# Kernel tuning notes

Hardware: AMD Instinct MI355X
Metric: run time of the kernel (lower is better)

Reference implementation:

```python
import jax, jax.numpy as jnp
import numpy as np

N_NODES = 50000
N_EDGES = 800000
N_GRAPHS = 128
IN_CH = 31
HID = 64
EPS = 1e-5


def _glorot(key, shape, scale=0.05):
    return jax.random.normal(key, shape, dtype=jnp.float32) * scale


def setup_inputs() -> dict:
    key = jax.random.key(0)
    ks = jax.random.split(key, 16)
    x = jax.random.normal(ks[0], (N_NODES, IN_CH), dtype=jnp.float32)
    edge_index = jax.random.randint(ks[1], (2, N_EDGES), 0, N_NODES, dtype=jnp.int32)
    batch = jnp.sort(jax.random.randint(ks[2], (N_NODES,), 0, N_GRAPHS, dtype=jnp.int32))
    params = {
        "t": jnp.ones((1,), dtype=jnp.float32),  # shared learnable softmax temperature
        "W1r": _glorot(ks[3], (HID, IN_CH)), "b1": jnp.zeros((HID,), jnp.float32), "W1s": _glorot(ks[4], (HID, IN_CH)),
        "W2r": _glorot(ks[5], (HID, HID)),  "b2": jnp.zeros((HID,), jnp.float32), "W2s": _glorot(ks[6], (HID, HID)),
        "W3r": _glorot(ks[7], (HID, HID)),  "b3": jnp.zeros((HID,), jnp.float32), "W3s": _glorot(ks[8], (HID, HID)),
        "Wl1": _glorot(ks[9], (2 * HID, 3 * HID)), "bl1": jnp.zeros((2 * HID,), jnp.float32),
        "Wl2": _glorot(ks[10], (HID // 2, 2 * HID)), "bl2": jnp.zeros((HID // 2,), jnp.float32),
    }
    return {"x": x, "edge_index": edge_index, "batch": batch, **params}


def _softmax_aggr(m, dst, t, n):
    # segment-softmax over incoming edges, per channel: alpha = softmax(t*m | dst)
    logits = m * t  # [E, C]
    mx = jax.ops.segment_max(logits, dst, num_segments=n)  # [N, C]
    e = jnp.exp(logits - mx[dst])
    denom = jax.ops.segment_sum(e, dst, num_segments=n)
    alpha = e / denom[dst]
    return jax.ops.segment_sum(m * alpha, dst, num_segments=n)  # [N, C]


def _graph_conv(x, src, dst, t, Wr, br, Ws):
    # PyG GraphConv: out = lin_rel(aggr_j x_j) + lin_root(x); lin_root has no bias
    m = x[src]  # gather [E, C]
    aggr = _softmax_aggr(m, dst, t, x.shape[0])
    return aggr @ Wr.T + br + x @ Ws.T


def _instance_norm(x):
    # torch InstanceNorm1d on [N, C] input -> normalize each row over feature dim
    mu = jnp.mean(x, axis=1, keepdims=True)
    var = jnp.mean((x - mu) ** 2, axis=1, keepdims=True)
    return (x - mu) / jnp.sqrt(var + EPS)


def reference(x, edge_index, batch, t, W1r, b1, W1s, W2r, b2, W2s, W3r, b3, W3s, Wl1, bl1, Wl2, bl2):
    src, dst = edge_index[0], edge_index[1]
    x1 = jax.nn.relu(_instance_norm(_graph_conv(x, src, dst, t, W1r, b1, W1s)))
    x2 = jax.nn.relu(_instance_norm(_graph_conv(x1, src, dst, t, W2r, b2, W2s)))
    x3 = jax.nn.relu(_instance_norm(_graph_conv(x2, src, dst, t, W3r, b3, W3s)))
    h1 = jax.ops.segment_max(x1, batch, num_segments=N_GRAPHS)
    h2 = jax.ops.segment_max(x2, batch, num_segments=N_GRAPHS)
    h3 = jax.ops.segment_max(x3, batch, num_segments=N_GRAPHS)
    h = jnp.concatenate([h1, h2, h3], axis=1)  # [G, 3*HID]
    z = jax.nn.relu(h @ Wl1.T + bl1)  # dropout is identity in eval mode
    z = z @ Wl2.T + bl2
    norm = jnp.maximum(jnp.linalg.norm(z, axis=1, keepdims=True), 1e-12)
    return z / norm
```

## Files before the change

### kernel.cpp

```cpp
#include <hip/hip_runtime.h>
#include <hip/hip_fp16.h>

#define N_NODES 50000
#define N_EDGES 800000
#define N_GRAPHS 128
#define IN_CH 31
#define HID 64

typedef __attribute__((ext_vector_type(8))) short short8;
typedef __attribute__((ext_vector_type(8))) unsigned short ushort8;
typedef __attribute__((ext_vector_type(4))) float floatx4;
typedef __attribute__((ext_vector_type(8))) _Float16 half8;

__device__ inline unsigned short f2h(float f) {
    __half h = __float2half_rn(f);
    return __half_as_ushort(h);
}
__device__ inline unsigned packh2(float a, float b) {
    __half2 h = __floats2half2_rn(a, b);
    return *(unsigned*)&h;
}
__device__ inline void pack4h(short* p, float4 v) {
    unsigned lo = packh2(v.x, v.y);
    unsigned hi = packh2(v.z, v.w);
    *(uint2*)p = make_uint2(lo, hi);
}
__device__ inline unsigned packEP(float E, float P) {
    return packh2(E, P);
}
__device__ inline float2 unpackEP(unsigned u) {
    __half2 h = *(__half2*)&u;
    return __half22float2(h);
}

__global__ void prep_kernel(const float* __restrict__ x, const float* __restrict__ tptr,
                            unsigned short* __restrict__ xh, unsigned* __restrict__ EP0,
                            int nN) {
    int i = blockIdx.x * 256 + threadIdx.x;
    if (i >= nN * 32) return;
    int node = i >> 5, c = i & 31;
    if (c < IN_CH) {
        float xv = x[node * IN_CH + c];
        xh[node * IN_CH + c] = f2h(xv);
        float tval = tptr[0];
        float E = __expf(tval * xv);
        EP0[i] = packEP(E, xv * E);
    } else {
        EP0[i] = 0;
    }
}


#define BKT_SHIFT 7
#define BKT_MAX 512
#define CHUNK 8192
#define CAP 2560

__global__ void bucket_scatter_kernel(const int* __restrict__ src,
                                      const int* __restrict__ dst,
                                      int* __restrict__ bucket_cnt,
                                      unsigned* __restrict__ ebuf, int e, int nb) {
    __shared__ int bins[BKT_MAX];
    __shared__ int base[BKT_MAX];
    __shared__ int lcur[BKT_MAX];
    int tid = threadIdx.x;
    int i0 = blockIdx.x * CHUNK;
    int i1 = i0 + CHUNK; if (i1 > e) i1 = e;
    for (int k = tid; k < nb; k += 256) { bins[k] = 0; lcur[k] = 0; }
    __syncthreads();
    for (int j = i0 + tid; j < i1; j += 256)
        atomicAdd(&bins[dst[j] >> BKT_SHIFT], 1);
    __syncthreads();
    for (int k = tid; k < nb; k += 256)
        if (bins[k]) base[k] = atomicAdd(&bucket_cnt[k], bins[k]);
    __syncthreads();
    for (int j = i0 + tid; j < i1; j += 256) {
        int ss = src[j], dd = dst[j];
        int b = dd >> BKT_SHIFT;
        int p = atomicAdd(&lcur[b], 1);
        ebuf[(size_t)b * CAP + base[b] + p] = (unsigned)ss | ((unsigned)(dd & 127) << 16);
    }
}

__global__ void bucket_csr_kernel(const unsigned* __restrict__ ebuf,
                                  const int* __restrict__ bucket_cnt,
                                  int* __restrict__ row_ptr, int* __restrict__ deg,
                                  int* __restrict__ csr_src, int nN) {
    __shared__ int nh[128];
    __shared__ int s[128];
    __shared__ int ncur[128];
    int tid = threadIdx.x;
    int b = blockIdx.x;
    int cnt = bucket_cnt[b];
    size_t boff = (size_t)b * CAP;
    int node0 = b << BKT_SHIFT;
    if (tid < 128) nh[tid] = 0;
    __syncthreads();
    for (int j = tid; j < cnt; j += 256)
        atomicAdd(&nh[ebuf[boff + j] >> 16], 1);
    __syncthreads();
    int v = (tid < 128) ? nh[tid] : 0;
    if (tid < 128) s[tid] = v;
    __syncthreads();
    for (int off = 1; off < 128; off <<= 1) {
        int u = (tid < 128 && tid >= off) ? s[tid - off] : 0;
        __syncthreads();
        if (tid < 128) s[tid] += u;
        __syncthreads();
    }
    if (tid < 128 && node0 + tid < nN) {
        int excl = (int)boff + s[tid] - v;
        row_ptr[node0 + tid] = excl;
        deg[node0 + tid] = v;
        ncur[tid] = excl;
    }
    __syncthreads();
    for (int j = tid; j < cnt; j += 256) {
        unsigned ed = ebuf[boff + j];
        int pos = atomicAdd(&ncur[ed >> 16], 1);
        csr_src[pos] = (int)(ed & 0xFFFF);
    }
}


template <int C_IN>
__global__ void __launch_bounds__(256, 8) aggr_kernel(
        const unsigned* __restrict__ EP, const unsigned short* __restrict__ xin,
        const float* __restrict__ tptr,
        const int* __restrict__ row_ptr, const int* __restrict__ deg,
        const int* __restrict__ csr_src,
        unsigned short* __restrict__ aRowsB, int n) {
    int w = threadIdx.x >> 6, l = threadIdx.x & 63;
    int d = blockIdx.x * 4 + w;
    if (d >= n) return;
    int beg = __builtin_amdgcn_readfirstlane(row_ptr[d]);
    int dg  = __builtin_amdgcn_readfirstlane(deg[d]);
    int end = beg + dg;
    int half = l >> 5;

    if constexpr (C_IN == 64) {
        int co = l & 31;
        float t2 = tptr[0] * 1.44269504f;
        const unsigned* Y = (const unsigned*)xin;
        float2 num2 = {0.f, 0.f}, den2 = {0.f, 0.f};
        int base = beg;
        for (; base + 64 <= end; base += 64) {
            int sidx = csr_src[base + l];
            #pragma unroll
            for (int j = 0; j < 64; j += 16) {
                unsigned v[8];
                #pragma unroll
                for (int p = 0; p < 8; ++p) {
                    int sa = __builtin_amdgcn_readlane(sidx, j + 2 * p);
                    int sb = __builtin_amdgcn_readlane(sidx, j + 2 * p + 1);
                    int s  = half ? sb : sa;
                    v[p] = Y[(size_t)s * 32 + co];
                }
                #pragma unroll
                for (int p = 0; p < 8; ++p) {
                    float2 y = __half22float2(*(__half2*)&v[p]);
                    float E0 = exp2f(t2 * y.x);
                    float E1 = exp2f(t2 * y.y);
                    den2.x += E0; num2.x = fmaf(y.x, E0, num2.x);
                    den2.y += E1; num2.y = fmaf(y.y, E1, num2.y);
                }
            }
        }
        int rem = end - base;
        if (rem > 0) {
            int sidx = csr_src[base + ((l < rem) ? l : 0)];
            for (int j = 0; j < rem; j += 16) {
                unsigned v[8];
                #pragma unroll
                for (int p = 0; p < 8; ++p) {
                    int ja = j + 2 * p;     if (ja >= rem) ja = rem - 1;
                    int jb = j + 2 * p + 1; if (jb >= rem) jb = rem - 1;
                    int sa = __builtin_amdgcn_readlane(sidx, ja);
                    int sb = __builtin_amdgcn_readlane(sidx, jb);
                    int s  = half ? sb : sa;
                    v[p] = Y[(size_t)s * 32 + co];
                }
                #pragma unroll
                for (int p = 0; p < 8; ++p) {
                    float m = (j + 2 * p + half < rem) ? 1.f : 0.f;
                    float2 y = __half22float2(*(__half2*)&v[p]);
                    float E0 = exp2f(t2 * y.x);
                    float E1 = exp2f(t2 * y.y);
                    den2.x = fmaf(E0, m, den2.x); num2.x = fmaf(y.x * E0, m, num2.x);
                    den2.y = fmaf(E1, m, den2.y); num2.y = fmaf(y.y * E1, m, num2.y);
                }
            }
        }
        num2.x += __shfl_xor(num2.x, 32);
        num2.y += __shfl_xor(num2.y, 32);
        den2.x += __shfl_xor(den2.x, 32);
        den2.y += __shfl_xor(den2.y, 32);
        float nx = __shfl(num2.x, l >> 1);
        float ny = __shfl(num2.y, l >> 1);
        float dx = __shfl(den2.x, l >> 1);
        float dy = __shfl(den2.y, l >> 1);
        float num = (l & 1) ? ny : nx;
        float den = (l & 1) ? dy : dx;
        float aggr = (dg > 0 && den > 0.f) ? num / den : 0.f;
        aRowsB[(size_t)d * 64 + l] = f2h(aggr);
    } else {
        int ch = l & 31;
        int chc = (ch < C_IN) ? ch : (C_IN - 1);
        float num = 0.f, den = 0.f;
        int base = beg;
        for (; base + 64 <= end; base += 64) {
            int sidx = csr_src[base + l];
            #pragma unroll
            for (int j = 0; j < 64; j += 16) {
                unsigned v[8];
                #pragma unroll
                for (int p = 0; p < 8; ++p) {
                    int sa = __builtin_amdgcn_readlane(sidx, j + 2 * p);
                    int sb = __builtin_amdgcn_readlane(sidx, j + 2 * p + 1);
                    int s  = half ? sb : sa;
                    v[p] = EP[(size_t)s * 32 + chc];
                }
                #pragma unroll
                for (int p = 0; p < 8; ++p) {
                    float2 e = unpackEP(v[p]);
                    den += e.x;
                    num += e.y;
                }
            }
        }
        int rem = end - base;
        if (rem > 0) {
            int sidx = csr_src[base + ((l < rem) ? l : 0)];
            for (int j = 0; j < rem; j += 16) {
                unsigned v[8];
                #pragma unroll
                for (int p = 0; p < 8; ++p) {
                    int ja = j + 2 * p;     if (ja >= rem) ja = rem - 1;
                    int jb = j + 2 * p + 1; if (jb >= rem) jb = rem - 1;
                    int sa = __builtin_amdgcn_readlane(sidx, ja);
                    int sb = __builtin_amdgcn_readlane(sidx, jb);
                    int s  = half ? sb : sa;
                    v[p] = EP[(size_t)s * 32 + chc];
                }
                #pragma unroll
                for (int p = 0; p < 8; ++p) {
                    float m = (j + 2 * p + half < rem) ? 1.f : 0.f;
                    float2 e = unpackEP(v[p]);
                    den = fmaf(e.x, m, den);
                    num = fmaf(e.y, m, num);
                }
            }
        }
        num += __shfl_xor(num, 32);
        den += __shfl_xor(den, 32);
        float aggr = (dg > 0 && den > 0.f) ? num / den : 0.f;
        unsigned short outv;
        if (l < C_IN)               outv = f2h(aggr);
        else if (l < 2 * C_IN)      outv = xin[(size_t)d * C_IN + (l - C_IN)];
        else                        outv = 0;
        aRowsB[(size_t)d * 64 + l] = outv;
    }
}


template <int C_IN, bool WY>
__global__ void __launch_bounds__(256, 4) transform_kernel(
        const unsigned short* __restrict__ aRowsB, const unsigned short* __restrict__ yprev,
        const int* __restrict__ batch,
        const float* __restrict__ Wr, const float* __restrict__ br,
        const float* __restrict__ Ws,
        unsigned short* __restrict__ yout,
        float* __restrict__ hmax, int n) {
    constexpr int K_TOT = (C_IN == 64) ? 128 : 64;
    constexpr int KP    = K_TOT + 8;
    constexpr int KS    = K_TOT / 32;
    constexpr int ABSH  = 2 * 64 * KP;
    constexpr int CSH   = 64 * 68 * 2;
    constexpr int SMSH  = (ABSH > CSH) ? ABSH : CSH;

    __shared__ short smem[SMSH];
    short* sA = smem;
    short* sB = smem + 64 * KP;
    float* sC = (float*)smem;

    int tid = threadIdx.x;
    int nb = blockIdx.x * 64;

    if constexpr (C_IN == 64) {
        for (int idx = tid; idx < 64 * 16; idx += 256) {
            int row = idx >> 4, c8 = idx & 15;
            int node = nb + row; if (node >= n) node = n - 1;
            ushort8 v = (c8 < 8) ? ((const ushort8*)(aRowsB + (size_t)node * 64))[c8]
                                 : ((const ushort8*)(yprev + (size_t)node * 64))[c8 - 8];
            *(ushort8*)&sA[row * KP + c8 * 8] = v;
        }
        for (int idx = tid; idx < 64 * 32; idx += 256) {
            int nr = idx >> 5, c4 = idx & 31;
            float4 v = (c4 < 16) ? ((const float4*)(Wr + nr * 64))[c4]
                                 : ((const float4*)(Ws + nr * 64))[c4 - 16];
            pack4h(&sB[nr * KP + c4 * 4], v);
        }
    } else {
        for (int idx = tid; idx < 64 * 8; idx += 256) {
            int row = idx >> 3, c8 = idx & 7;
            int node = nb + row; if (node >= n) node = n - 1;
            ushort8 v = ((const ushort8*)(aRowsB + (size_t)node * 64))[c8];
            *(ushort8*)&sA[row * KP + c8 * 8] = v;
        }
        for (int idx = tid; idx < 64 * 64; idx += 256) {
            int nr = idx >> 6, k = idx & 63;
            float v = (k < C_IN) ? Wr[nr * C_IN + k]
                    : (k < 2 * C_IN) ? Ws[nr * C_IN + (k - C_IN)] : 0.f;
            sB[nr * KP + k] = (short)f2h(v);
        }
    }
    __syncthreads();

    int w = tid >> 6, l = tid & 63;
    int m = l & 15;
    int q = l >> 4;
    floatx4 acc[4] = {{0.f,0.f,0.f,0.f},{0.f,0.f,0.f,0.f},
                      {0.f,0.f,0.f,0.f},{0.f,0.f,0.f,0.f}};
    const short* aBase = &sA[(w * 16 + m) * KP + q * 8];
    #pragma unroll 2
    for (int s = 0; s < KS; ++s) {
        half8 af = *(const half8*)(aBase + s * 32);
        #pragma unroll
        for (int t = 0; t < 4; ++t) {
            half8 bf = *(const half8*)&sB[(t * 16 + m) * KP + q * 8 + s * 32];
            acc[t] = __builtin_amdgcn_mfma_f32_16x16x32_f16(af, bf, acc[t], 0, 0, 0);
        }
    }

    __syncthreads();
    #pragma unroll
    for (int t = 0; t < 4; ++t)
        #pragma unroll
        for (int r = 0; r < 4; ++r)
            sC[(w * 16 + q * 4 + r) * 68 + t * 16 + m] = acc[t][r];
    __syncthreads();

    float bias = br[l];
    int gcur = -1;
    float rmax = 0.f;
    for (int i = 0; i < 16; ++i) {
        int j = w * 16 + i;
        int d = nb + j;
        if (d < n) {
            float a = sC[j * 68 + l] + bias;
            float s = a;
            for (int off = 32; off > 0; off >>= 1) s += __shfl_xor(s, off);
            float mu = s * (1.0f / 64.0f);
            float dc = a - mu;
            float s2 = dc * dc;
            for (int off = 32; off > 0; off >>= 1) s2 += __shfl_xor(s2, off);
            float var = s2 * (1.0f / 64.0f);
            float y = dc * rsqrtf(var + 1e-5f);
            y = fmaxf(y, 0.f);
            if constexpr (WY) {
                yout[(size_t)d * 64 + l] = f2h(y);
            }
            int g = __builtin_amdgcn_readfirstlane(batch[d]);
            if (g != gcur) {
                if (gcur >= 0)
                    atomicMax((int*)&hmax[gcur * 64 + l], __float_as_int(rmax));
                gcur = g;
                rmax = 0.f;
            }
            rmax = fmaxf(rmax, y);
        }
    }
    if (gcur >= 0)
        atomicMax((int*)&hmax[gcur * 64 + l], __float_as_int(rmax));
}


__global__ void mlp_kernel(const float* __restrict__ h,
                           const float* __restrict__ Wl1, const float* __restrict__ bl1,
                           const float* __restrict__ Wl2, const float* __restrict__ bl2,
                           float* __restrict__ out) {
    __shared__ float hrow[192];
    __shared__ float z1[128];
    __shared__ float z2[32];
    __shared__ float snorm;
    int g = blockIdx.x, tid = threadIdx.x;
    if (tid < 64) {
        hrow[tid]       = h[0 * N_GRAPHS * 64 + g * 64 + tid];
        hrow[64 + tid]  = h[1 * N_GRAPHS * 64 + g * 64 + tid];
        hrow[128 + tid] = h[2 * N_GRAPHS * 64 + g * 64 + tid];
    }
    __syncthreads();
    float acc = bl1[tid];
    #pragma unroll 8
    for (int c = 0; c < 192; ++c) acc = fmaf(hrow[c], Wl1[tid * 192 + c], acc);
    z1[tid] = fmaxf(acc, 0.f);
    __syncthreads();
    if (tid < 32) {
        float a2 = bl2[tid];
        #pragma unroll 8
        for (int c = 0; c < 128; ++c) a2 = fmaf(z1[c], Wl2[tid * 128 + c], a2);
        z2[tid] = a2;
    }
    __syncthreads();
    if (tid == 0) {
        float ss = 0.f;
        for (int i = 0; i < 32; ++i) ss += z2[i] * z2[i];
        snorm = fmaxf(sqrtf(ss), 1e-12f);
    }
    __syncthreads();
    if (tid < 32) out[g * 32 + tid] = z2[tid] / snorm;
}


extern "C" void kernel_launch(void* const* d_in, const int* in_sizes, int n_in,
                              void* d_out, int out_size, void* d_ws, size_t ws_size,
                              hipStream_t stream) {
    const float* x   = (const float*)d_in[0];
    const int* eidx  = (const int*)d_in[1];
    const int* batch = (const int*)d_in[2];
    const float* t   = (const float*)d_in[3];
    const float* W1r = (const float*)d_in[4];
    const float* b1  = (const float*)d_in[5];
    const float* W1s = (const float*)d_in[6];
    const float* W2r = (const float*)d_in[7];
    const float* b2  = (const float*)d_in[8];
    const float* W2s = (const float*)d_in[9];
    const float* W3r = (const float*)d_in[10];
    const float* b3  = (const float*)d_in[11];
    const float* W3s = (const float*)d_in[12];
    const float* Wl1 = (const float*)d_in[13];
    const float* bl1 = (const float*)d_in[14];
    const float* Wl2 = (const float*)d_in[15];
    const float* bl2 = (const float*)d_in[16];
    float* out = (float*)d_out;

    const int nE = in_sizes[1] / 2;
    const int nN = in_sizes[2];
    const int* src = eidx;
    const int* dst = eidx + nE;
    const int nb = (nN + 127) >> BKT_SHIFT;

    char* ws = (char*)d_ws;
    size_t off = 0;
    auto alloc = [&](size_t bytes) {
        char* p = ws + off;
        off = (off + bytes + 255) & ~(size_t)255;
        return p;
    };
    int*            bucket_cnt = (int*)alloc((size_t)BKT_MAX * 4);
    float*          h          = (float*)alloc((size_t)3 * N_GRAPHS * 64 * 4);
    int*            row_ptr    = (int*)alloc((size_t)nN * 4);
    int*            deg        = (int*)alloc((size_t)nN * 4);
    unsigned*       ebuf       = (unsigned*)alloc((size_t)nb * CAP * 4);
    int*            csr_src    = (int*)alloc((size_t)nb * CAP * 4);
    unsigned short* xh         = (unsigned short*)alloc((size_t)nN * IN_CH * 2);
    unsigned*       EP0        = (unsigned*)alloc((size_t)nN * 32 * 4);
    unsigned short* yAh        = (unsigned short*)alloc((size_t)nN * 64 * 2);
    unsigned short* yBh        = (unsigned short*)alloc((size_t)nN * 64 * 2);
    unsigned short* aRowsB     = (unsigned short*)alloc((size_t)nN * 64 * 2);

    const int nbChunk = (nE + CHUNK - 1) / CHUNK;

    hipMemsetAsync(bucket_cnt, 0,
                   (char*)(h + 3 * N_GRAPHS * 64) - (char*)bucket_cnt, stream);
    prep_kernel<<<(nN * 32 + 255) / 256, 256, 0, stream>>>(x, t, xh, EP0, nN);
    bucket_scatter_kernel<<<nbChunk, 256, 0, stream>>>(src, dst, bucket_cnt, ebuf, nE, nb);
    bucket_csr_kernel<<<nb, 256, 0, stream>>>(ebuf, bucket_cnt, row_ptr, deg, csr_src, nN);

    const int nbA = (nN + 3) / 4;
    const int nbT = (nN + 63) / 64;

    aggr_kernel<IN_CH><<<nbA, 256, 0, stream>>>(EP0, xh, t, row_ptr, deg, csr_src, aRowsB, nN);
    transform_kernel<IN_CH, true><<<nbT, 256, 0, stream>>>(
        aRowsB, nullptr, batch, W1r, b1, W1s, yAh, h + 0 * N_GRAPHS * 64, nN);

    aggr_kernel<HID><<<nbA, 256, 0, stream>>>(nullptr, yAh, t, row_ptr, deg, csr_src, aRowsB, nN);
    transform_kernel<HID, true><<<nbT, 256, 0, stream>>>(
        aRowsB, yAh, batch, W2r, b2, W2s, yBh, h + 1 * N_GRAPHS * 64, nN);

    aggr_kernel<HID><<<nbA, 256, 0, stream>>>(nullptr, yBh, t, row_ptr, deg, csr_src, aRowsB, nN);
    transform_kernel<HID, false><<<nbT, 256, 0, stream>>>(
        aRowsB, yBh, batch, W3r, b3, W3s, nullptr, h + 2 * N_GRAPHS * 64, nN);

    mlp_kernel<<<N_GRAPHS, 128, 0, stream>>>(h, Wl1, bl1, Wl2, bl2, out);
}
```

Measured before the change: 295.2 us.

## Precompute per-node exp and weighted values in transform epilogue for layers 2-3

The transform kernel now writes, for each node and channel, a packed fp16 pair of exp(t*y) and y*exp(t*y) alongside y. The 64-channel aggregation then gathers these precomputed pairs instead of recomputing exp per edge. The aggregation loop is unified into one generic path with 8-edge batches, one source node per load, and fdot2-based masked accumulation. The intent is to remove per-edge exp work, at the cost of doubling the gathered bytes per edge (4 bytes per channel instead of 2) and losing the two-edges-per-wave interleave.

```diff
diff --git a/kernel.cpp b/kernel.cpp
--- a/kernel.cpp
+++ b/kernel.cpp
@@ -11,6 +11,11 @@
 typedef __attribute__((ext_vector_type(8))) unsigned short ushort8;
 typedef __attribute__((ext_vector_type(4))) float floatx4;
 typedef __attribute__((ext_vector_type(8))) _Float16 half8;
+typedef __attribute__((ext_vector_type(2))) _Float16 half2v;
+
+#if __has_builtin(__builtin_amdgcn_fdot2)
+#define HAS_FDOT2 1
+#endif
 
 __device__ inline unsigned short f2h(float f) {
     __half h = __float2half_rn(f);
@@ -31,6 +36,9 @@
 __device__ inline float2 unpackEP(unsigned u) {
     __half2 h = *(__half2*)&u;
     return __half22float2(h);
+}
+__device__ inline half2v u2h2(unsigned u) {
+    return __builtin_bit_cast(half2v, u);
 }
 
 __global__ void prep_kernel(const float* __restrict__ x, const float* __restrict__ tptr,
@@ -126,134 +134,64 @@
 template <int C_IN>
 __global__ void __launch_bounds__(256, 8) aggr_kernel(
         const unsigned* __restrict__ EP, const unsigned short* __restrict__ xin,
-        const float* __restrict__ tptr,
         const int* __restrict__ row_ptr, const int* __restrict__ deg,
         const int* __restrict__ csr_src,
         unsigned short* __restrict__ aRowsB, int n) {
+    constexpr int ROWD = (C_IN == 64) ? 64 : 32;
     int w = threadIdx.x >> 6, l = threadIdx.x & 63;
     int d = blockIdx.x * 4 + w;
     if (d >= n) return;
     int beg = __builtin_amdgcn_readfirstlane(row_ptr[d]);
     int dg  = __builtin_amdgcn_readfirstlane(deg[d]);
     int end = beg + dg;
-    int half = l >> 5;
+    int cl = l & (ROWD - 1);
+
+    float den0 = 0.f, den1 = 0.f, num0 = 0.f, num1 = 0.f;
+    for (int base = beg; base < end; base += 64) {
+        int cend = base + 64; if (cend > end) cend = end;
+        int chunk = cend - base;
+        int sidx = csr_src[base + ((l < chunk) ? l : 0)];
+        for (int j0 = 0; j0 < chunk; j0 += 8) {
+            int jc = chunk - j0;
+            unsigned v[8];
+            #pragma unroll
+            for (int p = 0; p < 8; ++p) {
+                int jj = (p < jc) ? (j0 + p) : (chunk - 1);
+                int s  = __builtin_amdgcn_readlane(sidx, jj);
+                v[p] = EP[(size_t)s * ROWD + cl];
+            }
+            #pragma unroll
+            for (int p = 0; p < 8; ++p) {
+                bool live = (p < jc);
+#ifdef HAS_FDOT2
+                unsigned bE = live ? 0x00003C00u : 0u;
+                unsigned bP = live ? 0x3C000000u : 0u;
+                if (p & 1) {
+                    den1 = __builtin_amdgcn_fdot2(u2h2(v[p]), u2h2(bE), den1, false);
+                    num1 = __builtin_amdgcn_fdot2(u2h2(v[p]), u2h2(bP), num1, false);
+                } else {
+                    den0 = __builtin_amdgcn_fdot2(u2h2(v[p]), u2h2(bE), den0, false);
+                    num0 = __builtin_amdgcn_fdot2(u2h2(v[p]), u2h2(bP), num0, false);
+                }
+#else
+                float mm = live ? 1.f : 0.f;
+                float2 e = unpackEP(v[p]);
+                if (p & 1) {
+                    den1 = fmaf(e.x, mm, den1); num1 = fmaf(e.y, mm, num1);
+                } else {
+                    den0 = fmaf(e.x, mm, den0); num0 = fmaf(e.y, mm, num0);
+                }
+#endif
+            }
+        }
+    }
+    float den = den0 + den1;
+    float num = num0 + num1;
+    float aggr = (dg > 0 && den > 0.f) ? num / den : 0.f;
 
     if constexpr (C_IN == 64) {
-        int co = l & 31;
-        float t2 = tptr[0] * 1.44269504f;
-        const unsigned* Y = (const unsigned*)xin;
-        float2 num2 = {0.f, 0.f}, den2 = {0.f, 0.f};
-        int base = beg;
-        for (; base + 64 <= end; base += 64) {
-            int sidx = csr_src[base + l];
-            #pragma unroll
-            for (int j = 0; j < 64; j += 16) {
-                unsigned v[8];
-                #pragma unroll
-                for (int p = 0; p < 8; ++p) {
-                    int sa = __builtin_amdgcn_readlane(sidx, j + 2 * p);
-                    int sb = __builtin_amdgcn_readlane(sidx, j + 2 * p + 1);
-                    int s  = half ? sb : sa;
-                    v[p] = Y[(size_t)s * 32 + co];
-                }
-                #pragma unroll
-                for (int p = 0; p < 8; ++p) {
-                    float2 y = __half22float2(*(__half2*)&v[p]);
-                    float E0 = exp2f(t2 * y.x);
-                    float E1 = exp2f(t2 * y.y);
-                    den2.x += E0; num2.x = fmaf(y.x, E0, num2.x);
-                    den2.y += E1; num2.y = fmaf(y.y, E1, num2.y);
-                }
-            }
-        }
-        int rem = end - base;
-        if (rem > 0) {
-            int sidx = csr_src[base + ((l < rem) ? l : 0)];
-            for (int j = 0; j < rem; j += 16) {
-                unsigned v[8];
-                #pragma unroll
-                for (int p = 0; p < 8; ++p) {
-                    int ja = j + 2 * p;     if (ja >= rem) ja = rem - 1;
-                    int jb = j + 2 * p + 1; if (jb >= rem) jb = rem - 1;
-                    int sa = __builtin_amdgcn_readlane(sidx, ja);
-                    int sb = __builtin_amdgcn_readlane(sidx, jb);
-                    int s  = half ? sb : sa;
-                    v[p] = Y[(size_t)s * 32 + co];
-                }
-                #pragma unroll
-                for (int p = 0; p < 8; ++p) {
-                    float m = (j + 2 * p + half < rem) ? 1.f : 0.f;
-                    float2 y = __half22float2(*(__half2*)&v[p]);
-                    float E0 = exp2f(t2 * y.x);
-                    float E1 = exp2f(t2 * y.y);
-                    den2.x = fmaf(E0, m, den2.x); num2.x = fmaf(y.x * E0, m, num2.x);
-                    den2.y = fmaf(E1, m, den2.y); num2.y = fmaf(y.y * E1, m, num2.y);
-                }
-            }
-        }
-        num2.x += __shfl_xor(num2.x, 32);
-        num2.y += __shfl_xor(num2.y, 32);
-        den2.x += __shfl_xor(den2.x, 32);
-        den2.y += __shfl_xor(den2.y, 32);
-        float nx = __shfl(num2.x, l >> 1);
-        float ny = __shfl(num2.y, l >> 1);
-        float dx = __shfl(den2.x, l >> 1);
-        float dy = __shfl(den2.y, l >> 1);
-        float num = (l & 1) ? ny : nx;
-        float den = (l & 1) ? dy : dx;
-        float aggr = (dg > 0 && den > 0.f) ? num / den : 0.f;
         aRowsB[(size_t)d * 64 + l] = f2h(aggr);
     } else {
-        int ch = l & 31;
-        int chc = (ch < C_IN) ? ch : (C_IN - 1);
-        float num = 0.f, den = 0.f;
-        int base = beg;
-        for (; base + 64 <= end; base += 64) {
-            int sidx = csr_src[base + l];
-            #pragma unroll
-            for (int j = 0; j < 64; j += 16) {
-                unsigned v[8];
-                #pragma unroll
-                for (int p = 0; p < 8; ++p) {
-                    int sa = __builtin_amdgcn_readlane(sidx, j + 2 * p);
-                    int sb = __builtin_amdgcn_readlane(sidx, j + 2 * p + 1);
-                    int s  = half ? sb : sa;
-                    v[p] = EP[(size_t)s * 32 + chc];
-                }
-                #pragma unroll
-                for (int p = 0; p < 8; ++p) {
-                    float2 e = unpackEP(v[p]);
-                    den += e.x;
-                    num += e.y;
-                }
-            }
-        }
-        int rem = end - base;
-        if (rem > 0) {
-            int sidx = csr_src[base + ((l < rem) ? l : 0)];
-            for (int j = 0; j < rem; j += 16) {
-                unsigned v[8];
-                #pragma unroll
-                for (int p = 0; p < 8; ++p) {
-                    int ja = j + 2 * p;     if (ja >= rem) ja = rem - 1;
-                    int jb = j + 2 * p + 1; if (jb >= rem) jb = rem - 1;
-                    int sa = __builtin_amdgcn_readlane(sidx, ja);
-                    int sb = __builtin_amdgcn_readlane(sidx, jb);
-                    int s  = half ? sb : sa;
-                    v[p] = EP[(size_t)s * 32 + chc];
-                }
-                #pragma unroll
-                for (int p = 0; p < 8; ++p) {
-                    float m = (j + 2 * p + half < rem) ? 1.f : 0.f;
-                    float2 e = unpackEP(v[p]);
-                    den = fmaf(e.x, m, den);
-                    num = fmaf(e.y, m, num);
-                }
-            }
-        }
-        num += __shfl_xor(num, 32);
-        den += __shfl_xor(den, 32);
-        float aggr = (dg > 0 && den > 0.f) ? num / den : 0.f;
         unsigned short outv;
         if (l < C_IN)               outv = f2h(aggr);
         else if (l < 2 * C_IN)      outv = xin[(size_t)d * C_IN + (l - C_IN)];
@@ -263,13 +201,13 @@
 }
 
 
-template <int C_IN, bool WY>
+template <int C_IN, bool WEP>
 __global__ void __launch_bounds__(256, 4) transform_kernel(
         const unsigned short* __restrict__ aRowsB, const unsigned short* __restrict__ yprev,
         const int* __restrict__ batch,
         const float* __restrict__ Wr, const float* __restrict__ br,
-        const float* __restrict__ Ws,
-        unsigned short* __restrict__ yout,
+        const float* __restrict__ Ws, const float* __restrict__ tptr,
+        unsigned short* __restrict__ yout, unsigned* __restrict__ EPout,
         float* __restrict__ hmax, int n) {
     constexpr int K_TOT = (C_IN == 64) ? 128 : 64;
     constexpr int KP    = K_TOT + 8;
@@ -341,6 +279,8 @@
     __syncthreads();
 
     float bias = br[l];
+    float tval = 0.f;
+    if constexpr (WEP) tval = tptr[0];
     int gcur = -1;
     float rmax = 0.f;
     for (int i = 0; i < 16; ++i) {
@@ -357,8 +297,10 @@
             float var = s2 * (1.0f / 64.0f);
             float y = dc * rsqrtf(var + 1e-5f);
             y = fmaxf(y, 0.f);
-            if constexpr (WY) {
+            if constexpr (WEP) {
                 yout[(size_t)d * 64 + l] = f2h(y);
+                float E = __expf(tval * y);
+                EPout[(size_t)d * 64 + l] = packEP(E, y * E);
             }
             int g = __builtin_amdgcn_readfirstlane(batch[d]);
             if (g != gcur) {
@@ -455,6 +397,8 @@
     int*            csr_src    = (int*)alloc((size_t)nb * CAP * 4);
     unsigned short* xh         = (unsigned short*)alloc((size_t)nN * IN_CH * 2);
     unsigned*       EP0        = (unsigned*)alloc((size_t)nN * 32 * 4);
+    unsigned*       EPA        = (unsigned*)alloc((size_t)nN * 64 * 4);
+    unsigned*       EPB        = (unsigned*)alloc((size_t)nN * 64 * 4);
     unsigned short* yAh        = (unsigned short*)alloc((size_t)nN * 64 * 2);
     unsigned short* yBh        = (unsigned short*)alloc((size_t)nN * 64 * 2);
     unsigned short* aRowsB     = (unsigned short*)alloc((size_t)nN * 64 * 2);
@@ -470,17 +414,17 @@
     const int nbA = (nN + 3) / 4;
     const int nbT = (nN + 63) / 64;
 
-    aggr_kernel<IN_CH><<<nbA, 256, 0, stream>>>(EP0, xh, t, row_ptr, deg, csr_src, aRowsB, nN);
+    aggr_kernel<IN_CH><<<nbA, 256, 0, stream>>>(EP0, xh, row_ptr, deg, csr_src, aRowsB, nN);
     transform_kernel<IN_CH, true><<<nbT, 256, 0, stream>>>(
-        aRowsB, nullptr, batch, W1r, b1, W1s, yAh, h + 0 * N_GRAPHS * 64, nN);
-
-    aggr_kernel<HID><<<nbA, 256, 0, stream>>>(nullptr, yAh, t, row_ptr, deg, csr_src, aRowsB, nN);
+        aRowsB, nullptr, batch, W1r, b1, W1s, t, yAh, EPA, h + 0 * N_GRAPHS * 64, nN);
+
+    aggr_kernel<HID><<<nbA, 256, 0, stream>>>(EPA, nullptr, row_ptr, deg, csr_src, aRowsB, nN);
     transform_kernel<HID, true><<<nbT, 256, 0, stream>>>(
-        aRowsB, yAh, batch, W2r, b2, W2s, yBh, h + 1 * N_GRAPHS * 64, nN);
-
-    aggr_kernel<HID><<<nbA, 256, 0, stream>>>(nullptr, yBh, t, row_ptr, deg, csr_src, aRowsB, nN);
+        aRowsB, yAh, batch, W2r, b2, W2s, t, yBh, EPB, h + 1 * N_GRAPHS * 64, nN);
+
+    aggr_kernel<HID><<<nbA, 256, 0, stream>>>(EPB, nullptr, row_ptr, deg, csr_src, aRowsB, nN);
     transform_kernel<HID, false><<<nbT, 256, 0, stream>>>(
-        aRowsB, yBh, batch, W3r, b3, W3s, nullptr, h + 2 * N_GRAPHS * 64, nN);
+        aRowsB, yBh, batch, W3r, b3, W3s, t, nullptr, nullptr, h + 2 * N_GRAPHS * 64, nN);
 
     mlp_kernel<<<N_GRAPHS, 128, 0, stream>>>(h, Wl1, bl1, Wl2, bl2, out);
 }
```

Measured after the change: 270.1 us. 8.5% less time.
